# Optimization experiments

Hardware: AMD Instinct MI355X
Metric: run time of the kernel (lower is better)

The kernel has to match this reference:

```python
import jax, jax.numpy as jnp
import numpy as np

D_MODEL = 1024
N_HEADS = 16
D_HEAD = D_MODEL // N_HEADS


def setup_inputs() -> dict:
    key = jax.random.key(0)
    k1, k2, k3 = jax.random.split(key, 3)
    x = jax.random.normal(k1, (2, 2048, D_MODEL), dtype=jnp.float32)
    # Dense layer params (glorot-ish scale)
    W_qkv = jax.random.normal(k2, (D_MODEL, 3 * D_MODEL), dtype=jnp.float32) * (1.0 / np.sqrt(D_MODEL))
    b_qkv = jnp.zeros((3 * D_MODEL,), dtype=jnp.float32)
    W_proj = jax.random.normal(k3, (D_MODEL, D_MODEL), dtype=jnp.float32) * (1.0 / np.sqrt(D_MODEL))
    b_proj = jnp.zeros((D_MODEL,), dtype=jnp.float32)
    return {"x": x, "W_qkv": W_qkv, "b_qkv": b_qkv, "W_proj": W_proj, "b_proj": b_proj}


def reference(x, W_qkv, b_qkv, W_proj, b_proj):
    B, S, _ = x.shape
    qkv = x @ W_qkv + b_qkv                      # [B,S,3D]
    q, k, v = jnp.split(qkv, 3, axis=-1)
    # [B,S,D] -> [B,H,S,Dh]
    def to_heads(t):
        return t.reshape(B, S, N_HEADS, D_HEAD).transpose(0, 2, 1, 3)
    q, k, v = to_heads(q), to_heads(k), to_heads(v)
    scores = jnp.einsum('bhqd,bhkd->bhqk', q, k)  # [B,H,S,S]
    causal = jnp.tril(jnp.ones((S, S), dtype=bool))
    # NOTE: mask applied BEFORE scaling, matching the original module.
    scores = jnp.where(causal[None, None, :, :], scores, jnp.float32(-1e9))
    scaled = scores / jnp.sqrt(jnp.float32(D_HEAD))
    attn = jax.nn.softmax(scaled, axis=-1)
    ctx = jnp.einsum('bhqk,bhkd->bhqd', attn, v)  # [B,H,S,Dh]
    ctx = ctx.transpose(0, 2, 1, 3).reshape(B, S, D_MODEL)
    return ctx @ W_proj + b_proj
```

## Files before the change

### kernel.cpp

```cpp
#include <hip/hip_runtime.h>
#include <stdint.h>

typedef __attribute__((ext_vector_type(8))) short short8;
typedef __attribute__((ext_vector_type(4))) float f32x4;

#define QSCALE 0.18033688011112043f

__device__ __forceinline__ unsigned short f2b(float f) {
  union { float f; uint32_t u; } v; v.f = f;
  uint32_t u = v.u;
  u = u + 0x7fffu + ((u >> 16) & 1u);
  return (unsigned short)(u >> 16);
}
__device__ __forceinline__ unsigned int cvtpk(float lo, float hi) {
  unsigned int r;
  asm("v_cvt_pk_bf16_f32 %0, %1, %2" : "=v"(r) : "v"(lo), "v"(hi));
  return r;
}
__device__ __forceinline__ void gload16(const void* g, void* lds) {
  __builtin_amdgcn_global_load_lds((const __attribute__((address_space(1))) void*)g,
                                   (__attribute__((address_space(3))) void*)lds, 16, 0, 0);
}

__global__ __launch_bounds__(256) void cvt_f32_bf16(const float* __restrict__ in,
                                                    unsigned short* __restrict__ out, int n) {
  int i = (blockIdx.x * 256 + threadIdx.x) * 4;
  if (i < n) {
    float4 v = *(const float4*)(in + i);
    ushort4 o;
    o.x = f2b(v.x); o.y = f2b(v.y); o.z = f2b(v.z); o.w = f2b(v.w);
    *(ushort4*)(out + i) = o;
  }
}

__global__ __launch_bounds__(256) void transposeW(const float* __restrict__ W,
                                                  unsigned short* __restrict__ Wt,
                                                  int K, int N, float scale, int scaleRows) {
  __shared__ float tile[32][33];
  int x0 = blockIdx.x * 32, y0 = blockIdx.y * 32;
  int tx = threadIdx.x, ty = threadIdx.y;
  #pragma unroll
  for (int j = 0; j < 4; ++j)
    tile[ty + j * 8][tx] = W[(size_t)(y0 + ty + j * 8) * N + x0 + tx];
  __syncthreads();
  #pragma unroll
  for (int j = 0; j < 4; ++j) {
    int orow = x0 + ty + j * 8;
    float s = (orow < scaleRows) ? scale : 1.0f;
    Wt[(size_t)orow * K + y0 + tx] = f2b(tile[tx][ty + j * 8] * s);
  }
}

template<bool OUTF32>
__global__ __launch_bounds__(256) void gemm_bt(const unsigned short* __restrict__ A,
                                               const unsigned short* __restrict__ Bt,
                                               const float* __restrict__ bias,
                                               void* __restrict__ outp,
                                               int M, int N, int K,
                                               float bscale, int bscaleN, int mtiles) {
  __shared__ unsigned short As[2][128 * 64];
  __shared__ unsigned short Bs[2][128 * 64];
  const int t = threadIdx.x;
  const int lane = t & 63;
  const int w = t >> 6;
  const int wm = w >> 1, wn = w & 1;

  const int cpx = gridDim.x >> 3;
  const int swz = (blockIdx.x & 7) * cpx + (blockIdx.x >> 3);
  const int m0 = (swz % mtiles) * 128;
  const int n0 = (swz / mtiles) * 128;

  const f32x4 zero = {0.f, 0.f, 0.f, 0.f};
  f32x4 acc[4][4];
  #pragma unroll
  for (int i = 0; i < 4; ++i)
    #pragma unroll
    for (int j = 0; j < 4; ++j) acc[i][j] = zero;

  const int cl = lane & 15, g = lane >> 4;
  const int srow = t >> 3;
  const int sch  = (t & 7) ^ (srow & 7);

  auto stage = [&](int k0, int buf) {
    #pragma unroll
    for (int r = 0; r < 4; ++r) {
      int row = r * 32 + srow;
      gload16(A  + (size_t)(m0 + row) * K + k0 + sch * 8, (char*)As[buf] + r * 4096 + t * 16);
      gload16(Bt + (size_t)(n0 + row) * K + k0 + sch * 8, (char*)Bs[buf] + r * 4096 + t * 16);
    }
  };

  stage(0, 0);
  __syncthreads();

  const int nk = K >> 6;
  for (int ki = 0; ki < nk; ++ki) {
    const int cur = ki & 1;
    if (ki + 1 < nk) stage((ki + 1) << 6, cur ^ 1);
    char* AsB = (char*)As[cur];
    char* BsB = (char*)Bs[cur];
    #pragma unroll
    for (int kk = 0; kk < 2; ++kk) {
      short8 af[4], bfr[4];
      #pragma unroll
      for (int f = 0; f < 4; ++f) {
        int arow = wm * 64 + f * 16 + cl;
        int brow = wn * 64 + f * 16 + cl;
        af[f]  = *(const short8*)(AsB + ((arow * 128 + kk * 64 + g * 16) ^ ((cl & 7) << 4)));
        bfr[f] = *(const short8*)(BsB + ((brow * 128 + kk * 64 + g * 16) ^ ((cl & 7) << 4)));
      }
      #pragma unroll
      for (int fm = 0; fm < 4; ++fm)
        #pragma unroll
        for (int fn = 0; fn < 4; ++fn)
          acc[fm][fn] = __builtin_amdgcn_mfma_f32_16x16x32_bf16(af[fm], bfr[fn], acc[fm][fn], 0, 0, 0);
    }
    __syncthreads();
  }

  #pragma unroll
  for (int fn = 0; fn < 4; ++fn) {
    int col = n0 + wn * 64 + fn * 16 + cl;
    float bv = bias[col] * ((col < bscaleN) ? bscale : 1.0f);
    #pragma unroll
    for (int fm = 0; fm < 4; ++fm) {
      int rbase = m0 + wm * 64 + fm * 16 + g * 4;
      #pragma unroll
      for (int r = 0; r < 4; ++r) {
        float vout = acc[fm][fn][r] + bv;
        if (OUTF32) ((float*)outp)[(size_t)(rbase + r) * N + col] = vout;
        else ((unsigned short*)outp)[(size_t)(rbase + r) * N + col] = f2b(vout);
      }
    }
  }
}

__global__ __launch_bounds__(256) void transposeV(const unsigned short* __restrict__ qkv,
                                                  unsigned short* __restrict__ Vt) {
  __shared__ unsigned short tile[64][72];
  const int bh = blockIdx.y, b = bh >> 4, h = bh & 15;
  const int s0 = blockIdx.x * 64;
  const int t = threadIdx.x;
  #pragma unroll
  for (int i = 0; i < 2; ++i) {
    int c = t + i * 256;
    int srow = c >> 3, d0 = (c & 7) * 8;
    short8 v = *(const short8*)(qkv + (size_t)(b * 2048 + s0 + srow) * 3072 + 2048 + h * 64 + d0);
    *(short8*)(&tile[srow][d0]) = v;
  }
  __syncthreads();
  #pragma unroll
  for (int i = 0; i < 2; ++i) {
    int c = t + i * 256;
    int d = c >> 3, sb = (c & 7) * 8;
    short8 o;
    #pragma unroll
    for (int j = 0; j < 8; ++j) o[j] = tile[sb + j][d];
    *(short8*)(Vt + (size_t)(bh * 64 + d) * 2048 + s0 + sb) = o;
  }
}

__device__ __forceinline__ void attn_tile(const short8 ak[4][2], const short8 av[4][2],
                                          const short8 a5[2], const short8 bq[2],
                                          char* Pbuf, f32x4 o[4], f32x4& o5,
                                          float& m, bool maskIter, int cl, int g, int w) {
  f32x4 st[4];
  #pragma unroll
  for (int tt = 0; tt < 4; ++tt) st[tt] = (f32x4){0.f, 0.f, 0.f, 0.f};
  __builtin_amdgcn_s_setprio(1);
  #pragma unroll
  for (int kk = 0; kk < 2; ++kk)
    #pragma unroll
    for (int tt = 0; tt < 4; ++tt)
      st[tt] = __builtin_amdgcn_mfma_f32_16x16x32_bf16(ak[tt][kk], bq[kk], st[tt], 0, 0, 0);
  __builtin_amdgcn_s_setprio(0);

  float z[4][4];
  #pragma unroll
  for (int tt = 0; tt < 4; ++tt)
    #pragma unroll
    for (int r = 0; r < 4; ++r) z[tt][r] = st[tt][r];
  if (maskIter) {
    int q_loc = w * 16 + cl;
    #pragma unroll
    for (int tt = 0; tt < 4; ++tt)
      #pragma unroll
      for (int r = 0; r < 4; ++r)
        if (tt * 16 + 4 * g + r > q_loc) z[tt][r] = -1e30f;
  }
  float cm = z[0][0];
  #pragma unroll
  for (int tt = 0; tt < 4; ++tt)
    #pragma unroll
    for (int r = 0; r < 4; ++r) cm = fmaxf(cm, z[tt][r]);
  cm = fmaxf(cm, __shfl_xor(cm, 16));
  cm = fmaxf(cm, __shfl_xor(cm, 32));

  if (!__all(cm <= m + 8.f)) {
    float mn = fmaxf(m, cm);
    float alpha = exp2f(m - mn);
    m = mn;
    #pragma unroll
    for (int c = 0; c < 4; ++c)
      #pragma unroll
      for (int r = 0; r < 4; ++r) o[c][r] *= alpha;
    o5[0] *= alpha;
  }

  #pragma unroll
  for (int tt = 0; tt < 4; ++tt) {
    float p0 = exp2f(z[tt][0] - m), p1 = exp2f(z[tt][1] - m);
    float p2 = exp2f(z[tt][2] - m), p3 = exp2f(z[tt][3] - m);
    uint2 val;
    val.x = cvtpk(p0, p1);
    val.y = cvtpk(p2, p3);
    *(uint2*)(Pbuf + ((cl * 128 + tt * 32 + g * 8) ^ ((cl & 7) << 4))) = val;
  }
  short8 bp[2];
  #pragma unroll
  for (int kk = 0; kk < 2; ++kk)
    bp[kk] = *(const short8*)(Pbuf + ((cl * 128 + kk * 64 + g * 16) ^ ((cl & 7) << 4)));

  __builtin_amdgcn_s_setprio(1);
  #pragma unroll
  for (int kk = 0; kk < 2; ++kk) {
    #pragma unroll
    for (int c = 0; c < 4; ++c)
      o[c] = __builtin_amdgcn_mfma_f32_16x16x32_bf16(av[c][kk], bp[kk], o[c], 0, 0, 0);
    o5 = __builtin_amdgcn_mfma_f32_16x16x32_bf16(a5[kk], bp[kk], o5, 0, 0, 0);
  }
  __builtin_amdgcn_s_setprio(0);
}

__global__ __launch_bounds__(256, 2) void attn_mfma2(const unsigned short* __restrict__ qkv,
                                                     const unsigned short* __restrict__ Vt,
                                                     unsigned short* __restrict__ ctx) {
  const int p  = blockIdx.x;
  const int bh = blockIdx.y;
  const int b = bh >> 4, h = bh & 15;
  const int qtA = p, qtB = 31 - p;
  const int t = threadIdx.x;
  const int l = t & 63;
  const int w = t >> 6;
  const int cl = l & 15;
  const int g  = l >> 4;

  __shared__ unsigned short Ks[2][64 * 64];
  __shared__ unsigned short Vs[2][64 * 64];
  __shared__ unsigned short Ps[4][2][16 * 64];
  __shared__ unsigned short Ones[16 * 64];

  char* PbA = (char*)(&Ps[w][0][0]);
  char* PbB = (char*)(&Ps[w][1][0]);
  char* OnB = (char*)Ones;

  const size_t kbase  = (size_t)(b * 2048) * 3072 + 1024 + h * 64;
  const size_t vtbase = (size_t)(bh * 64) * 2048;

  auto stage = [&](int jt, int buf) {
    #pragma unroll
    for (int i = 0; i < 2; ++i) {
      int row = i * 32 + w * 8 + (l >> 3);
      int ch  = (l & 7) ^ (l >> 3);
      gload16(qkv + kbase + (size_t)(jt * 64 + row) * 3072 + ch * 8,
              (char*)Ks[buf] + i * 4096 + w * 1024);
      gload16(Vt + vtbase + (size_t)row * 2048 + jt * 64 + ch * 8,
              (char*)Vs[buf] + i * 4096 + w * 1024);
    }
  };

  {
    int row = t >> 4;
    int c4  = (t & 15) * 4;
    unsigned short vv = (row == 0) ? (unsigned short)0x3F80 : (unsigned short)0;
    ushort4 ov = {vv, vv, vv, vv};
    *(ushort4*)(OnB + ((row * 128 + c4 * 2) ^ ((row & 7) << 4))) = ov;
  }

  stage(0, 0);
  __syncthreads();

  short8 a5[2];
  #pragma unroll
  for (int kk = 0; kk < 2; ++kk)
    a5[kk] = *(const short8*)(OnB + ((cl * 128 + kk * 64 + g * 16) ^ ((cl & 7) << 4)));

  short8 bqA[2], bqB[2];
  {
    const unsigned short* qa = qkv + (size_t)(b * 2048 + qtA * 64 + w * 16 + cl) * 3072 + h * 64 + g * 8;
    bqA[0] = *(const short8*)(qa);
    bqA[1] = *(const short8*)(qa + 32);
    const unsigned short* qb = qkv + (size_t)(b * 2048 + qtB * 64 + w * 16 + cl) * 3072 + h * 64 + g * 8;
    bqB[0] = *(const short8*)(qb);
    bqB[1] = *(const short8*)(qb + 32);
  }

  f32x4 oA[4], oB[4], o5A, o5B;
  #pragma unroll
  for (int c = 0; c < 4; ++c) { oA[c] = (f32x4){0.f,0.f,0.f,0.f}; oB[c] = (f32x4){0.f,0.f,0.f,0.f}; }
  o5A = (f32x4){0.f,0.f,0.f,0.f};
  o5B = (f32x4){0.f,0.f,0.f,0.f};
  float mA = -1e30f, mB = -1e30f;

  for (int jt = 0; jt <= qtB; ++jt) {
    const int cur = jt & 1;
    if (jt < qtB) stage(jt + 1, cur ^ 1);
    char* KsB = (char*)Ks[cur];
    char* VsB = (char*)Vs[cur];

    short8 ak[4][2];
    #pragma unroll
    for (int tt = 0; tt < 4; ++tt)
      #pragma unroll
      for (int kk = 0; kk < 2; ++kk)
        ak[tt][kk] = *(const short8*)(KsB + (((tt * 16 + cl) * 128 + kk * 64 + g * 16) ^ ((cl & 7) << 4)));
    short8 av[4][2];
    #pragma unroll
    for (int c = 0; c < 4; ++c)
      #pragma unroll
      for (int kk = 0; kk < 2; ++kk)
        av[c][kk] = *(const short8*)(VsB + (((c * 16 + cl) * 128 + kk * 64 + g * 16) ^ ((cl & 7) << 4)));

    if (jt <= qtA) attn_tile(ak, av, a5, bqA, PbA, oA, o5A, mA, jt == qtA, cl, g, w);
    attn_tile(ak, av, a5, bqB, PbB, oB, o5B, mB, jt == qtB, cl, g, w);

    __syncthreads();
  }

  {
    float lsum = __shfl(o5A[0], cl);
    float inv = 1.f / lsum;
    unsigned short* crow = ctx + (size_t)(b * 2048 + qtA * 64 + w * 16 + cl) * 1024 + h * 64 + g * 4;
    #pragma unroll
    for (int c = 0; c < 4; ++c) {
      uint2 val;
      val.x = cvtpk(oA[c][0] * inv, oA[c][1] * inv);
      val.y = cvtpk(oA[c][2] * inv, oA[c][3] * inv);
      *(uint2*)(crow + c * 16) = val;
    }
  }
  {
    float lsum = __shfl(o5B[0], cl);
    float inv = 1.f / lsum;
    unsigned short* crow = ctx + (size_t)(b * 2048 + qtB * 64 + w * 16 + cl) * 1024 + h * 64 + g * 4;
    #pragma unroll
    for (int c = 0; c < 4; ++c) {
      uint2 val;
      val.x = cvtpk(oB[c][0] * inv, oB[c][1] * inv);
      val.y = cvtpk(oB[c][2] * inv, oB[c][3] * inv);
      *(uint2*)(crow + c * 16) = val;
    }
  }
}

extern "C" void kernel_launch(void* const* d_in, const int* in_sizes, int n_in,
                              void* d_out, int out_size, void* d_ws, size_t ws_size,
                              hipStream_t stream) {
  const float* x     = (const float*)d_in[0];
  const float* Wqkv  = (const float*)d_in[1];
  const float* bqkv  = (const float*)d_in[2];
  const float* Wproj = (const float*)d_in[3];
  const float* bproj = (const float*)d_in[4];
  float* out = (float*)d_out;

  char* ws = (char*)d_ws;
  unsigned short* xb     = (unsigned short*)(ws);
  unsigned short* wqkvT  = (unsigned short*)(ws + 8388608);
  unsigned short* wprojT = (unsigned short*)(ws + 14680064);
  unsigned short* qkv    = (unsigned short*)(ws + 16777216);
  unsigned short* ctx    = (unsigned short*)(ws + 41943040);
  unsigned short* vt     = (unsigned short*)(ws + 50331648);

  cvt_f32_bf16<<<4096, 256, 0, stream>>>(x, xb, 4096 * 1024);

  dim3 tb(32, 8);
  transposeW<<<dim3(3072 / 32, 1024 / 32), tb, 0, stream>>>(Wqkv, wqkvT, 1024, 3072, QSCALE, 1024);
  transposeW<<<dim3(1024 / 32, 1024 / 32), tb, 0, stream>>>(Wproj, wprojT, 1024, 1024, 1.0f, 0);

  gemm_bt<false><<<768, 256, 0, stream>>>(xb, wqkvT, bqkv, qkv, 4096, 3072, 1024,
                                          QSCALE, 1024, 32);

  transposeV<<<dim3(32, 32), 256, 0, stream>>>(qkv, vt);

  attn_mfma2<<<dim3(16, 32), 256, 0, stream>>>(qkv, vt, ctx);

  gemm_bt<true><<<256, 256, 0, stream>>>(ctx, wprojT, bproj, out, 4096, 1024, 1024,
                                         1.0f, 0, 32);
}
```

Before: 197.7 us.

## Fuse V transpose into QKV GEMM epilogue, split attention per q-tile, narrow proj GEMM tile

```diff
diff --git a/kernel.cpp b/kernel.cpp
--- a/kernel.cpp
+++ b/kernel.cpp
@@ -51,15 +51,17 @@
   }
 }
 
-template<bool OUTF32>
-__global__ __launch_bounds__(256) void gemm_bt(const unsigned short* __restrict__ A,
-                                               const unsigned short* __restrict__ Bt,
-                                               const float* __restrict__ bias,
-                                               void* __restrict__ outp,
-                                               int M, int N, int K,
-                                               float bscale, int bscaleN, int mtiles) {
+template<bool OUTF32, int BN>
+__global__ __launch_bounds__(256, 3) void gemm_bt(const unsigned short* __restrict__ A,
+                                                  const unsigned short* __restrict__ Bt,
+                                                  const float* __restrict__ bias,
+                                                  void* __restrict__ outp,
+                                                  unsigned short* __restrict__ vtOut,
+                                                  int M, int N, int K,
+                                                  float bscale, int bscaleN, int mtiles) {
+  constexpr int FN = BN / 32;
   __shared__ unsigned short As[2][128 * 64];
-  __shared__ unsigned short Bs[2][128 * 64];
+  __shared__ unsigned short Bs[2][BN * 64];
   const int t = threadIdx.x;
   const int lane = t & 63;
   const int w = t >> 6;
@@ -68,14 +70,14 @@
   const int cpx = gridDim.x >> 3;
   const int swz = (blockIdx.x & 7) * cpx + (blockIdx.x >> 3);
   const int m0 = (swz % mtiles) * 128;
-  const int n0 = (swz / mtiles) * 128;
+  const int n0 = (swz / mtiles) * BN;
 
   const f32x4 zero = {0.f, 0.f, 0.f, 0.f};
-  f32x4 acc[4][4];
+  f32x4 acc[4][FN];
   #pragma unroll
   for (int i = 0; i < 4; ++i)
     #pragma unroll
-    for (int j = 0; j < 4; ++j) acc[i][j] = zero;
+    for (int j = 0; j < FN; ++j) acc[i][j] = zero;
 
   const int cl = lane & 15, g = lane >> 4;
   const int srow = t >> 3;
@@ -83,11 +85,13 @@
 
   auto stage = [&](int k0, int buf) {
     #pragma unroll
-    for (int r = 0; r < 4; ++r) {
-      int row = r * 32 + srow;
-      gload16(A  + (size_t)(m0 + row) * K + k0 + sch * 8, (char*)As[buf] + r * 4096 + t * 16);
-      gload16(Bt + (size_t)(n0 + row) * K + k0 + sch * 8, (char*)Bs[buf] + r * 4096 + t * 16);
-    }
+    for (int r = 0; r < 4; ++r)
+      gload16(A + (size_t)(m0 + r * 32 + srow) * K + k0 + sch * 8,
+              (char*)As[buf] + r * 4096 + t * 16);
+    #pragma unroll
+    for (int r = 0; r < BN / 32; ++r)
+      gload16(Bt + (size_t)(n0 + r * 32 + srow) * K + k0 + sch * 8,
+              (char*)Bs[buf] + r * 4096 + t * 16);
   };
 
   stage(0, 0);
@@ -101,144 +105,67 @@
     char* BsB = (char*)Bs[cur];
     #pragma unroll
     for (int kk = 0; kk < 2; ++kk) {
-      short8 af[4], bfr[4];
+      short8 af[4], bfr[FN];
       #pragma unroll
       for (int f = 0; f < 4; ++f) {
         int arow = wm * 64 + f * 16 + cl;
-        int brow = wn * 64 + f * 16 + cl;
         af[f]  = *(const short8*)(AsB + ((arow * 128 + kk * 64 + g * 16) ^ ((cl & 7) << 4)));
+      }
+      #pragma unroll
+      for (int f = 0; f < FN; ++f) {
+        int brow = wn * (BN / 2) + f * 16 + cl;
         bfr[f] = *(const short8*)(BsB + ((brow * 128 + kk * 64 + g * 16) ^ ((cl & 7) << 4)));
       }
       #pragma unroll
       for (int fm = 0; fm < 4; ++fm)
         #pragma unroll
-        for (int fn = 0; fn < 4; ++fn)
+        for (int fn = 0; fn < FN; ++fn)
           acc[fm][fn] = __builtin_amdgcn_mfma_f32_16x16x32_bf16(af[fm], bfr[fn], acc[fm][fn], 0, 0, 0);
     }
     __syncthreads();
   }
 
-  #pragma unroll
-  for (int fn = 0; fn < 4; ++fn) {
-    int col = n0 + wn * 64 + fn * 16 + cl;
+  const bool vpath = (!OUTF32) && (vtOut != nullptr) && (n0 >= 2048);
+  #pragma unroll
+  for (int fn = 0; fn < FN; ++fn) {
+    int col = n0 + wn * (BN / 2) + fn * 16 + cl;
     float bv = bias[col] * ((col < bscaleN) ? bscale : 1.0f);
-    #pragma unroll
-    for (int fm = 0; fm < 4; ++fm) {
-      int rbase = m0 + wm * 64 + fm * 16 + g * 4;
-      #pragma unroll
-      for (int r = 0; r < 4; ++r) {
-        float vout = acc[fm][fn][r] + bv;
-        if (OUTF32) ((float*)outp)[(size_t)(rbase + r) * N + col] = vout;
-        else ((unsigned short*)outp)[(size_t)(rbase + r) * N + col] = f2b(vout);
+    if (vpath) {
+      int hcol = col - 2048;
+      size_t vrow = (size_t)hcol * 2048;
+      #pragma unroll
+      for (int fm = 0; fm < 4; ++fm) {
+        int rbase = m0 + wm * 64 + fm * 16 + g * 4;
+        int b = rbase >> 11, s = rbase & 2047;
+        ushort4 ov;
+        ov.x = f2b(acc[fm][fn][0] + bv);
+        ov.y = f2b(acc[fm][fn][1] + bv);
+        ov.z = f2b(acc[fm][fn][2] + bv);
+        ov.w = f2b(acc[fm][fn][3] + bv);
+        *(ushort4*)(vtOut + (size_t)b * 1024 * 2048 + vrow + s) = ov;
       }
-    }
-  }
-}
-
-__global__ __launch_bounds__(256) void transposeV(const unsigned short* __restrict__ qkv,
-                                                  unsigned short* __restrict__ Vt) {
-  __shared__ unsigned short tile[64][72];
-  const int bh = blockIdx.y, b = bh >> 4, h = bh & 15;
-  const int s0 = blockIdx.x * 64;
-  const int t = threadIdx.x;
-  #pragma unroll
-  for (int i = 0; i < 2; ++i) {
-    int c = t + i * 256;
-    int srow = c >> 3, d0 = (c & 7) * 8;
-    short8 v = *(const short8*)(qkv + (size_t)(b * 2048 + s0 + srow) * 3072 + 2048 + h * 64 + d0);
-    *(short8*)(&tile[srow][d0]) = v;
-  }
-  __syncthreads();
-  #pragma unroll
-  for (int i = 0; i < 2; ++i) {
-    int c = t + i * 256;
-    int d = c >> 3, sb = (c & 7) * 8;
-    short8 o;
-    #pragma unroll
-    for (int j = 0; j < 8; ++j) o[j] = tile[sb + j][d];
-    *(short8*)(Vt + (size_t)(bh * 64 + d) * 2048 + s0 + sb) = o;
-  }
-}
-
-__device__ __forceinline__ void attn_tile(const short8 ak[4][2], const short8 av[4][2],
-                                          const short8 a5[2], const short8 bq[2],
-                                          char* Pbuf, f32x4 o[4], f32x4& o5,
-                                          float& m, bool maskIter, int cl, int g, int w) {
-  f32x4 st[4];
-  #pragma unroll
-  for (int tt = 0; tt < 4; ++tt) st[tt] = (f32x4){0.f, 0.f, 0.f, 0.f};
-  __builtin_amdgcn_s_setprio(1);
-  #pragma unroll
-  for (int kk = 0; kk < 2; ++kk)
-    #pragma unroll
-    for (int tt = 0; tt < 4; ++tt)
-      st[tt] = __builtin_amdgcn_mfma_f32_16x16x32_bf16(ak[tt][kk], bq[kk], st[tt], 0, 0, 0);
-  __builtin_amdgcn_s_setprio(0);
-
-  float z[4][4];
-  #pragma unroll
-  for (int tt = 0; tt < 4; ++tt)
-    #pragma unroll
-    for (int r = 0; r < 4; ++r) z[tt][r] = st[tt][r];
-  if (maskIter) {
-    int q_loc = w * 16 + cl;
-    #pragma unroll
-    for (int tt = 0; tt < 4; ++tt)
-      #pragma unroll
-      for (int r = 0; r < 4; ++r)
-        if (tt * 16 + 4 * g + r > q_loc) z[tt][r] = -1e30f;
-  }
-  float cm = z[0][0];
-  #pragma unroll
-  for (int tt = 0; tt < 4; ++tt)
-    #pragma unroll
-    for (int r = 0; r < 4; ++r) cm = fmaxf(cm, z[tt][r]);
-  cm = fmaxf(cm, __shfl_xor(cm, 16));
-  cm = fmaxf(cm, __shfl_xor(cm, 32));
-
-  if (!__all(cm <= m + 8.f)) {
-    float mn = fmaxf(m, cm);
-    float alpha = exp2f(m - mn);
-    m = mn;
-    #pragma unroll
-    for (int c = 0; c < 4; ++c)
-      #pragma unroll
-      for (int r = 0; r < 4; ++r) o[c][r] *= alpha;
-    o5[0] *= alpha;
-  }
-
-  #pragma unroll
-  for (int tt = 0; tt < 4; ++tt) {
-    float p0 = exp2f(z[tt][0] - m), p1 = exp2f(z[tt][1] - m);
-    float p2 = exp2f(z[tt][2] - m), p3 = exp2f(z[tt][3] - m);
-    uint2 val;
-    val.x = cvtpk(p0, p1);
-    val.y = cvtpk(p2, p3);
-    *(uint2*)(Pbuf + ((cl * 128 + tt * 32 + g * 8) ^ ((cl & 7) << 4))) = val;
-  }
-  short8 bp[2];
-  #pragma unroll
-  for (int kk = 0; kk < 2; ++kk)
-    bp[kk] = *(const short8*)(Pbuf + ((cl * 128 + kk * 64 + g * 16) ^ ((cl & 7) << 4)));
-
-  __builtin_amdgcn_s_setprio(1);
-  #pragma unroll
-  for (int kk = 0; kk < 2; ++kk) {
-    #pragma unroll
-    for (int c = 0; c < 4; ++c)
-      o[c] = __builtin_amdgcn_mfma_f32_16x16x32_bf16(av[c][kk], bp[kk], o[c], 0, 0, 0);
-    o5 = __builtin_amdgcn_mfma_f32_16x16x32_bf16(a5[kk], bp[kk], o5, 0, 0, 0);
-  }
-  __builtin_amdgcn_s_setprio(0);
-}
-
-__global__ __launch_bounds__(256, 2) void attn_mfma2(const unsigned short* __restrict__ qkv,
+    } else {
+      #pragma unroll
+      for (int fm = 0; fm < 4; ++fm) {
+        int rbase = m0 + wm * 64 + fm * 16 + g * 4;
+        #pragma unroll
+        for (int r = 0; r < 4; ++r) {
+          float vout = acc[fm][fn][r] + bv;
+          if (OUTF32) ((float*)outp)[(size_t)(rbase + r) * N + col] = vout;
+          else ((unsigned short*)outp)[(size_t)(rbase + r) * N + col] = f2b(vout);
+        }
+      }
+    }
+  }
+}
+
+__global__ __launch_bounds__(256, 3) void attn_mfma3(const unsigned short* __restrict__ qkv,
                                                      const unsigned short* __restrict__ Vt,
                                                      unsigned short* __restrict__ ctx) {
-  const int p  = blockIdx.x;
-  const int bh = blockIdx.y;
+  const int idx = blockIdx.x;
+  const int bh = ((idx & 7) << 2) | ((idx >> 3) & 3);
+  const int qt = 31 - (idx >> 5);
   const int b = bh >> 4, h = bh & 15;
-  const int qtA = p, qtB = 31 - p;
   const int t = threadIdx.x;
   const int l = t & 63;
   const int w = t >> 6;
@@ -247,11 +174,10 @@
 
   __shared__ unsigned short Ks[2][64 * 64];
   __shared__ unsigned short Vs[2][64 * 64];
-  __shared__ unsigned short Ps[4][2][16 * 64];
+  __shared__ unsigned short Ps[4][16 * 64];
   __shared__ unsigned short Ones[16 * 64];
 
-  char* PbA = (char*)(&Ps[w][0][0]);
-  char* PbB = (char*)(&Ps[w][1][0]);
+  char* Pbuf = (char*)(&Ps[w][0]);
   char* OnB = (char*)Ones;
 
   const size_t kbase  = (size_t)(b * 2048) * 3072 + 1024 + h * 64;
@@ -285,26 +211,22 @@
   for (int kk = 0; kk < 2; ++kk)
     a5[kk] = *(const short8*)(OnB + ((cl * 128 + kk * 64 + g * 16) ^ ((cl & 7) << 4)));
 
-  short8 bqA[2], bqB[2];
+  short8 bq[2];
   {
-    const unsigned short* qa = qkv + (size_t)(b * 2048 + qtA * 64 + w * 16 + cl) * 3072 + h * 64 + g * 8;
-    bqA[0] = *(const short8*)(qa);
-    bqA[1] = *(const short8*)(qa + 32);
-    const unsigned short* qb = qkv + (size_t)(b * 2048 + qtB * 64 + w * 16 + cl) * 3072 + h * 64 + g * 8;
-    bqB[0] = *(const short8*)(qb);
-    bqB[1] = *(const short8*)(qb + 32);
-  }
-
-  f32x4 oA[4], oB[4], o5A, o5B;
-  #pragma unroll
-  for (int c = 0; c < 4; ++c) { oA[c] = (f32x4){0.f,0.f,0.f,0.f}; oB[c] = (f32x4){0.f,0.f,0.f,0.f}; }
-  o5A = (f32x4){0.f,0.f,0.f,0.f};
-  o5B = (f32x4){0.f,0.f,0.f,0.f};
-  float mA = -1e30f, mB = -1e30f;
-
-  for (int jt = 0; jt <= qtB; ++jt) {
+    const unsigned short* qp = qkv + (size_t)(b * 2048 + qt * 64 + w * 16 + cl) * 3072 + h * 64 + g * 8;
+    bq[0] = *(const short8*)(qp);
+    bq[1] = *(const short8*)(qp + 32);
+  }
+
+  f32x4 o[4], o5;
+  #pragma unroll
+  for (int c = 0; c < 4; ++c) o[c] = (f32x4){0.f, 0.f, 0.f, 0.f};
+  o5 = (f32x4){0.f, 0.f, 0.f, 0.f};
+  float m = -1e30f;
+
+  for (int jt = 0; jt <= qt; ++jt) {
     const int cur = jt & 1;
-    if (jt < qtB) stage(jt + 1, cur ^ 1);
+    if (jt < qt) stage(jt + 1, cur ^ 1);
     char* KsB = (char*)Ks[cur];
     char* VsB = (char*)Vs[cur];
 
@@ -321,35 +243,85 @@
       for (int kk = 0; kk < 2; ++kk)
         av[c][kk] = *(const short8*)(VsB + (((c * 16 + cl) * 128 + kk * 64 + g * 16) ^ ((cl & 7) << 4)));
 
-    if (jt <= qtA) attn_tile(ak, av, a5, bqA, PbA, oA, o5A, mA, jt == qtA, cl, g, w);
-    attn_tile(ak, av, a5, bqB, PbB, oB, o5B, mB, jt == qtB, cl, g, w);
+    f32x4 st[4];
+    #pragma unroll
+    for (int tt = 0; tt < 4; ++tt) st[tt] = (f32x4){0.f, 0.f, 0.f, 0.f};
+    __builtin_amdgcn_s_setprio(1);
+    #pragma unroll
+    for (int kk = 0; kk < 2; ++kk)
+      #pragma unroll
+      for (int tt = 0; tt < 4; ++tt)
+        st[tt] = __builtin_amdgcn_mfma_f32_16x16x32_bf16(ak[tt][kk], bq[kk], st[tt], 0, 0, 0);
+    __builtin_amdgcn_s_setprio(0);
+
+    float z[4][4];
+    #pragma unroll
+    for (int tt = 0; tt < 4; ++tt)
+      #pragma unroll
+      for (int r = 0; r < 4; ++r) z[tt][r] = st[tt][r];
+    if (jt == qt) {
+      int q_loc = w * 16 + cl;
+      #pragma unroll
+      for (int tt = 0; tt < 4; ++tt)
+        #pragma unroll
+        for (int r = 0; r < 4; ++r)
+          if (tt * 16 + 4 * g + r > q_loc) z[tt][r] = -1e30f;
+    }
+    float m0a = fmaxf(fmaxf(z[0][0], z[0][1]), fmaxf(z[0][2], z[0][3]));
+    float m1a = fmaxf(fmaxf(z[1][0], z[1][1]), fmaxf(z[1][2], z[1][3]));
+    float m2a = fmaxf(fmaxf(z[2][0], z[2][1]), fmaxf(z[2][2], z[2][3]));
+    float m3a = fmaxf(fmaxf(z[3][0], z[3][1]), fmaxf(z[3][2], z[3][3]));
+    float cm = fmaxf(fmaxf(m0a, m1a), fmaxf(m2a, m3a));
+    cm = fmaxf(cm, __shfl_xor(cm, 16));
+    cm = fmaxf(cm, __shfl_xor(cm, 32));
+
+    if (!__all(cm <= m + 8.f)) {
+      float mn = fmaxf(m, cm);
+      float alpha = exp2f(m - mn);
+      m = mn;
+      #pragma unroll
+      for (int c = 0; c < 4; ++c)
+        #pragma unroll
+        for (int r = 0; r < 4; ++r) o[c][r] *= alpha;
+      o5[0] *= alpha;
+    }
+
+    #pragma unroll
+    for (int tt = 0; tt < 4; ++tt) {
+      float p0 = exp2f(z[tt][0] - m), p1 = exp2f(z[tt][1] - m);
+      float p2 = exp2f(z[tt][2] - m), p3 = exp2f(z[tt][3] - m);
+      uint2 val;
+      val.x = cvtpk(p0, p1);
+      val.y = cvtpk(p2, p3);
+      *(uint2*)(Pbuf + ((cl * 128 + tt * 32 + g * 8) ^ ((cl & 7) << 4))) = val;
+    }
+    short8 bp[2];
+    #pragma unroll
+    for (int kk = 0; kk < 2; ++kk)
+      bp[kk] = *(const short8*)(Pbuf + ((cl * 128 + kk * 64 + g * 16) ^ ((cl & 7) << 4)));
+
+    __builtin_amdgcn_s_setprio(1);
+    #pragma unroll
+    for (int kk = 0; kk < 2; ++kk) {
+      #pragma unroll
+      for (int c = 0; c < 4; ++c)
+        o[c] = __builtin_amdgcn_mfma_f32_16x16x32_bf16(av[c][kk], bp[kk], o[c], 0, 0, 0);
+      o5 = __builtin_amdgcn_mfma_f32_16x16x32_bf16(a5[kk], bp[kk], o5, 0, 0, 0);
+    }
+    __builtin_amdgcn_s_setprio(0);
 
     __syncthreads();
   }
 
-  {
-    float lsum = __shfl(o5A[0], cl);
-    float inv = 1.f / lsum;
-    unsigned short* crow = ctx + (size_t)(b * 2048 + qtA * 64 + w * 16 + cl) * 1024 + h * 64 + g * 4;
-    #pragma unroll
-    for (int c = 0; c < 4; ++c) {
-      uint2 val;
-      val.x = cvtpk(oA[c][0] * inv, oA[c][1] * inv);
-      val.y = cvtpk(oA[c][2] * inv, oA[c][3] * inv);
-      *(uint2*)(crow + c * 16) = val;
-    }
-  }
-  {
-    float lsum = __shfl(o5B[0], cl);
-    float inv = 1.f / lsum;
-    unsigned short* crow = ctx + (size_t)(b * 2048 + qtB * 64 + w * 16 + cl) * 1024 + h * 64 + g * 4;
-    #pragma unroll
-    for (int c = 0; c < 4; ++c) {
-      uint2 val;
-      val.x = cvtpk(oB[c][0] * inv, oB[c][1] * inv);
-      val.y = cvtpk(oB[c][2] * inv, oB[c][3] * inv);
-      *(uint2*)(crow + c * 16) = val;
-    }
+  float lsum = __shfl(o5[0], cl);
+  float inv = 1.f / lsum;
+  unsigned short* crow = ctx + (size_t)(b * 2048 + qt * 64 + w * 16 + cl) * 1024 + h * 64 + g * 4;
+  #pragma unroll
+  for (int c = 0; c < 4; ++c) {
+    uint2 val;
+    val.x = cvtpk(o[c][0] * inv, o[c][1] * inv);
+    val.y = cvtpk(o[c][2] * inv, o[c][3] * inv);
+    *(uint2*)(crow + c * 16) = val;
   }
 }
 
@@ -377,13 +349,11 @@
   transposeW<<<dim3(3072 / 32, 1024 / 32), tb, 0, stream>>>(Wqkv, wqkvT, 1024, 3072, QSCALE, 1024);
   transposeW<<<dim3(1024 / 32, 1024 / 32), tb, 0, stream>>>(Wproj, wprojT, 1024, 1024, 1.0f, 0);
 
-  gemm_bt<false><<<768, 256, 0, stream>>>(xb, wqkvT, bqkv, qkv, 4096, 3072, 1024,
-                                          QSCALE, 1024, 32);
-
-  transposeV<<<dim3(32, 32), 256, 0, stream>>>(qkv, vt);
-
-  attn_mfma2<<<dim3(16, 32), 256, 0, stream>>>(qkv, vt, ctx);
-
-  gemm_bt<true><<<256, 256, 0, stream>>>(ctx, wprojT, bproj, out, 4096, 1024, 1024,
-                                         1.0f, 0, 32);
-}
+  gemm_bt<false, 128><<<768, 256, 0, stream>>>(xb, wqkvT, bqkv, qkv, vt,
+                                               4096, 3072, 1024, QSCALE, 1024, 32);
+
+  attn_mfma3<<<1024, 256, 0, stream>>>(qkv, vt, ctx);
+
+  gemm_bt<true, 64><<<512, 256, 0, stream>>>(ctx, wprojT, bproj, out, nullptr,
+                                             4096, 1024, 1024, 1.0f, 0, 32);
+}
```

After: 191.8 us. 1.03x faster.
